# Kernel optimization log

Measured on AMD Instinct MI355X. Metric: run time of the kernel, lower is better.

## Reference

```python
import jax, jax.numpy as jnp
import numpy as np

B, N, D = 1024, 1024, 256


def _mlp(x, w1, b1, w2, b2):
    return jax.nn.relu(x @ w1.T + b1) @ w2.T + b2


def _gru_cell(x, h, wih, whh, bih, bhh):
    gi = x @ wih.T + bih            # [*, 3D]
    gh = h @ whh.T + bhh            # [*, 3D]
    ir, iz, in_ = jnp.split(gi, 3, axis=-1)
    hr, hz, hn = jnp.split(gh, 3, axis=-1)
    r = jax.nn.sigmoid(ir + hr)
    z = jax.nn.sigmoid(iz + hz)
    n = jnp.tanh(in_ + r * hn)
    return (1.0 - z) * n + z * h


def setup_inputs() -> dict:
    key = jax.random.key(0)
    ks = jax.random.split(key, 20)
    s = 0.05
    inp = {
        "memory": jax.random.normal(ks[0], (N, D), jnp.float32),
        "source": jax.random.randint(ks[1], (B, 1), 0, N, jnp.int64 if jax.config.read('jax_enable_x64') else jnp.int32),
        "target": jax.random.randint(ks[2], (B, 1), 0, N, jnp.int64 if jax.config.read('jax_enable_x64') else jnp.int32),
        "delta_t_vec": jax.random.normal(ks[3], (B, N, D), jnp.float32),
        # src_mlp: Linear(3D->D), ReLU, Linear(D->D)
        "src_w1": jax.random.normal(ks[4], (D, 3 * D), jnp.float32) * s,
        "src_b1": jax.random.normal(ks[5], (D,), jnp.float32) * s,
        "src_w2": jax.random.normal(ks[6], (D, D), jnp.float32) * s,
        "src_b2": jax.random.normal(ks[7], (D,), jnp.float32) * s,
        # tar_mlp
        "tar_w1": jax.random.normal(ks[8], (D, 3 * D), jnp.float32) * s,
        "tar_b1": jax.random.normal(ks[9], (D,), jnp.float32) * s,
        "tar_w2": jax.random.normal(ks[10], (D, D), jnp.float32) * s,
        "tar_b2": jax.random.normal(ks[11], (D,), jnp.float32) * s,
        # GRUCell(D, D)
        "gru_wih": jax.random.normal(ks[12], (3 * D, D), jnp.float32) * s,
        "gru_whh": jax.random.normal(ks[13], (3 * D, D), jnp.float32) * s,
        "gru_bih": jax.random.normal(ks[14], (3 * D,), jnp.float32) * s,
        "gru_bhh": jax.random.normal(ks[15], (3 * D,), jnp.float32) * s,
    }
    return inp


def reference(memory, source, target, delta_t_vec,
              src_w1, src_b1, src_w2, src_b2,
              tar_w1, tar_b1, tar_w2, tar_b2,
              gru_wih, gru_whh, gru_bih, gru_bhh):
    b = source.shape[0]
    n_nodes = memory.shape[0]
    src = source[:, 0]
    tgt = target[:, 0]
    bidx = jnp.arange(b)

    src_mem = memory[src]                      # [B,D]
    tgt_mem = memory[tgt]                      # [B,D]
    src_dt = delta_t_vec[bidx, src]            # [B,D]
    tgt_dt = delta_t_vec[bidx, tgt]            # [B,D]

    src_msg = _mlp(jnp.concatenate([src_mem, tgt_mem, src_dt], -1),
                   src_w1, src_b1, src_w2, src_b2)
    tgt_msg = _mlp(jnp.concatenate([tgt_mem, src_mem, tgt_dt], -1),
                   tar_w1, tar_b1, tar_w2, tar_b2)

    # scatter_mean over concatenated (src, tgt) node ids == unique + scatter_mean by inverse index
    nodes = jnp.concatenate([src, tgt], 0)     # [2B]
    msgs = jnp.concatenate([src_msg, tgt_msg], 0)  # [2B,D]
    sums = jax.ops.segment_sum(msgs, nodes, num_segments=n_nodes)      # [N,D]
    cnts = jax.ops.segment_sum(jnp.ones((2 * b,), msgs.dtype), nodes,
                               num_segments=n_nodes)                    # [N]
    agg = sums / jnp.maximum(cnts, 1.0)[:, None]

    new_mem = _gru_cell(agg, memory, gru_wih, gru_whh, gru_bih, gru_bhh)
    touched = (cnts > 0)[:, None]
    return jnp.where(touched, new_mem, memory)
```

## Files before the change

### kernel.cpp

```cpp
#include <hip/hip_runtime.h>
#include <cmath>

typedef unsigned short u16;
typedef unsigned int u32;

using bf16x8 = __attribute__((ext_vector_type(8))) __bf16;
using f32x4  = __attribute__((ext_vector_type(4))) float;

__device__ __forceinline__ u16 f2bf(float f) {
  union { float f; u32 i; } v; v.f = f;
  u32 u = v.i;
  return (u16)((u + 0x7FFFu + ((u >> 16) & 1u)) >> 16);
}

__device__ __forceinline__ uint4 cvt8(const float* __restrict__ p) {
  float4 a = *(const float4*)p;
  float4 b = *(const float4*)(p + 4);
  union { u16 h[8]; uint4 v; } r;
  r.h[0] = f2bf(a.x); r.h[1] = f2bf(a.y); r.h[2] = f2bf(a.z); r.h[3] = f2bf(a.w);
  r.h[4] = f2bf(b.x); r.h[5] = f2bf(b.y); r.h[6] = f2bf(b.z); r.h[7] = f2bf(b.w);
  return r.v;
}
__device__ __forceinline__ uint4 cvt8s(const float* __restrict__ p, float s) {
  float4 a = *(const float4*)p;
  float4 b = *(const float4*)(p + 4);
  union { u16 h[8]; uint4 v; } r;
  r.h[0] = f2bf(a.x * s); r.h[1] = f2bf(a.y * s); r.h[2] = f2bf(a.z * s); r.h[3] = f2bf(a.w * s);
  r.h[4] = f2bf(b.x * s); r.h[5] = f2bf(b.y * s); r.h[6] = f2bf(b.z * s); r.h[7] = f2bf(b.w * s);
  return r.v;
}

#define LDS_STRIDE 72

__global__ __launch_bounds__(256) void k_mlp1(
    const float* __restrict__ memory, const int* __restrict__ src,
    const int* __restrict__ tgt, const float* __restrict__ delta,
    const float* __restrict__ w1s, const float* __restrict__ b1s,
    const float* __restrict__ w1t, const float* __restrict__ b1t,
    u16* __restrict__ H) {
  __shared__ __align__(16) u16 As[64 * LDS_STRIDE];
  __shared__ __align__(16) u16 Bs[64 * LDS_STRIDE];
  const int m0 = blockIdx.x * 64;
  const int n0 = blockIdx.y * 64;
  const int side = (m0 >= 1024);
  const float* __restrict__ W  = side ? w1t : w1s;
  const float* __restrict__ b1 = side ? b1t : b1s;
  const int tid = threadIdx.x;
  const int wv = tid >> 6, lane = tid & 63, quad = lane >> 4, l16 = lane & 15;

  f32x4 acc[4];
#pragma unroll
  for (int i = 0; i < 4; ++i) acc[i] = (f32x4){0.f, 0.f, 0.f, 0.f};

  for (int kc = 0; kc < 768; kc += 64) {
    __syncthreads();
#pragma unroll
    for (int it = 0; it < 2; ++it) {
      int c2 = tid + it * 256;
      int r = c2 >> 3, c8 = (c2 & 7) << 3;
      int k = kc + c8;
      int m = m0 + r, b = m & 1023;
      int ia = side ? tgt[b] : src[b];
      const float* p;
      int seg = k >> 8, kk = k & 255;
      if (seg == 0) {
        p = memory + ia * 256 + kk;
      } else if (seg == 1) {
        int ib = side ? src[b] : tgt[b];
        p = memory + ib * 256 + kk;
      } else {
        p = delta + ((size_t)(b * 1024 + ia)) * 256 + kk;
      }
      *(uint4*)&As[r * LDS_STRIDE + c8] = cvt8(p);
      *(uint4*)&Bs[r * LDS_STRIDE + c8] = cvt8(W + (n0 + r) * 768 + k);
    }
    __syncthreads();
#pragma unroll
    for (int ks = 0; ks < 64; ks += 32) {
      bf16x8 af = *(const bf16x8*)&As[(wv * 16 + l16) * LDS_STRIDE + ks + quad * 8];
#pragma unroll
      for (int nt = 0; nt < 4; ++nt) {
        bf16x8 bf = *(const bf16x8*)&Bs[(nt * 16 + l16) * LDS_STRIDE + ks + quad * 8];
        acc[nt] = __builtin_amdgcn_mfma_f32_16x16x32_bf16(af, bf, acc[nt], 0, 0, 0);
      }
    }
  }
#pragma unroll
  for (int nt = 0; nt < 4; ++nt) {
    int n = n0 + nt * 16 + l16;
    float bias = b1[n];
#pragma unroll
    for (int r = 0; r < 4; ++r) {
      int m = m0 + wv * 16 + quad * 4 + r;
      float v = acc[nt][r] + bias;
      H[m * 256 + n] = f2bf(v > 0.f ? v : 0.f);
    }
  }
}

__global__ __launch_bounds__(256) void k_mlp2_scatter(
    const u16* __restrict__ H, const int* __restrict__ src,
    const int* __restrict__ tgt,
    const float* __restrict__ w2s, const float* __restrict__ b2s,
    const float* __restrict__ w2t, const float* __restrict__ b2t,
    float* __restrict__ sums, float* __restrict__ cnt) {
  __shared__ __align__(16) u16 As[64 * LDS_STRIDE];
  __shared__ __align__(16) u16 Bs[64 * LDS_STRIDE];
  const int m0 = blockIdx.x * 64;
  const int n0 = blockIdx.y * 64;
  const int side = (m0 >= 1024);
  const float* __restrict__ W  = side ? w2t : w2s;
  const float* __restrict__ b2 = side ? b2t : b2s;
  const int tid = threadIdx.x;
  const int wv = tid >> 6, lane = tid & 63, quad = lane >> 4, l16 = lane & 15;

  f32x4 acc[4];
#pragma unroll
  for (int i = 0; i < 4; ++i) acc[i] = (f32x4){0.f, 0.f, 0.f, 0.f};

  for (int kc = 0; kc < 256; kc += 64) {
    __syncthreads();
#pragma unroll
    for (int it = 0; it < 2; ++it) {
      int c2 = tid + it * 256;
      int r = c2 >> 3, c8 = (c2 & 7) << 3;
      int k = kc + c8;
      *(uint4*)&As[r * LDS_STRIDE + c8] = *(const uint4*)(H + (m0 + r) * 256 + k);
      *(uint4*)&Bs[r * LDS_STRIDE + c8] = cvt8(W + (n0 + r) * 256 + k);
    }
    __syncthreads();
#pragma unroll
    for (int ks = 0; ks < 64; ks += 32) {
      bf16x8 af = *(const bf16x8*)&As[(wv * 16 + l16) * LDS_STRIDE + ks + quad * 8];
#pragma unroll
      for (int nt = 0; nt < 4; ++nt) {
        bf16x8 bf = *(const bf16x8*)&Bs[(nt * 16 + l16) * LDS_STRIDE + ks + quad * 8];
        acc[nt] = __builtin_amdgcn_mfma_f32_16x16x32_bf16(af, bf, acc[nt], 0, 0, 0);
      }
    }
  }
#pragma unroll
  for (int nt = 0; nt < 4; ++nt) {
    int n = n0 + nt * 16 + l16;
    float bias = b2[n];
#pragma unroll
    for (int r = 0; r < 4; ++r) {
      int m = m0 + wv * 16 + quad * 4 + r;
      int b = m & 1023;
      int node = side ? tgt[b] : src[b];
      atomicAdd(&sums[node * 256 + n], acc[nt][r] + bias);
    }
  }
  if (blockIdx.y == 0 && l16 == 0) {
#pragma unroll
    for (int r = 0; r < 4; ++r) {
      int m = m0 + wv * 16 + quad * 4 + r;
      int b = m & 1023;
      int node = side ? tgt[b] : src[b];
      atomicAdd(&cnt[node], 1.0f);
    }
  }
}

__global__ __launch_bounds__(256) void k_gru_gemm(
    const float* __restrict__ sums, const float* __restrict__ cnt,
    const float* __restrict__ memory,
    const float* __restrict__ wih, const float* __restrict__ whh,
    const float* __restrict__ bih, const float* __restrict__ bhh,
    float* __restrict__ G) {
  __shared__ __align__(16) u16 As[64 * LDS_STRIDE];
  __shared__ __align__(16) u16 Bs[64 * LDS_STRIDE];
  const int m0 = blockIdx.x * 64;
  const int n0 = blockIdx.y * 64;
  const bool ghreg = (n0 >= 768);
  const int tid = threadIdx.x;
  const int wv = tid >> 6, lane = tid & 63, quad = lane >> 4, l16 = lane & 15;

  f32x4 acc[4];
#pragma unroll
  for (int i = 0; i < 4; ++i) acc[i] = (f32x4){0.f, 0.f, 0.f, 0.f};

  for (int kc = 0; kc < 256; kc += 64) {
    __syncthreads();
#pragma unroll
    for (int it = 0; it < 2; ++it) {
      int c2 = tid + it * 256;
      int r = c2 >> 3, c8 = (c2 & 7) << 3;
      int k = kc + c8;
      int m = m0 + r;
      if (ghreg) {
        *(uint4*)&As[r * LDS_STRIDE + c8] = cvt8(memory + m * 256 + k);
      } else {
        float scale = 1.0f / fmaxf(cnt[m], 1.0f);
        *(uint4*)&As[r * LDS_STRIDE + c8] = cvt8s(sums + m * 256 + k, scale);
      }
      int ng = n0 + r;
      const float* Wr = (ng < 768) ? (wih + ng * 256) : (whh + (ng - 768) * 256);
      *(uint4*)&Bs[r * LDS_STRIDE + c8] = cvt8(Wr + k);
    }
    __syncthreads();
#pragma unroll
    for (int ks = 0; ks < 64; ks += 32) {
      bf16x8 af = *(const bf16x8*)&As[(wv * 16 + l16) * LDS_STRIDE + ks + quad * 8];
#pragma unroll
      for (int nt = 0; nt < 4; ++nt) {
        bf16x8 bf = *(const bf16x8*)&Bs[(nt * 16 + l16) * LDS_STRIDE + ks + quad * 8];
        acc[nt] = __builtin_amdgcn_mfma_f32_16x16x32_bf16(af, bf, acc[nt], 0, 0, 0);
      }
    }
  }
#pragma unroll
  for (int nt = 0; nt < 4; ++nt) {
    int ng = n0 + nt * 16 + l16;
    float bias = (ng < 768) ? bih[ng] : bhh[ng - 768];
#pragma unroll
    for (int r = 0; r < 4; ++r) {
      int m = m0 + wv * 16 + quad * 4 + r;
      G[m * 1536 + ng] = acc[nt][r] + bias;
    }
  }
}

__global__ __launch_bounds__(256) void k_gru_epi(
    const float* __restrict__ G, const float* __restrict__ cnt,
    const float* __restrict__ memory, float* __restrict__ out) {
  int gid = blockIdx.x * 256 + threadIdx.x;
  int m = gid >> 8, d = gid & 255;
  const float* g = G + m * 1536;
  float ir = g[d], iz = g[256 + d], in_ = g[512 + d];
  float hr = g[768 + d], hz = g[1024 + d], hn = g[1280 + d];
  float r = 1.f / (1.f + expf(-(ir + hr)));
  float z = 1.f / (1.f + expf(-(iz + hz)));
  float nn = tanhf(in_ + r * hn);
  float h = memory[gid];
  float nv = (1.f - z) * nn + z * h;
  out[gid] = (cnt[m] > 0.f) ? nv : h;
}

extern "C" void kernel_launch(void* const* d_in, const int* in_sizes, int n_in,
                              void* d_out, int out_size, void* d_ws, size_t ws_size,
                              hipStream_t stream) {
  const float* memory = (const float*)d_in[0];
  const int*   src    = (const int*)d_in[1];
  const int*   tgt    = (const int*)d_in[2];
  const float* delta  = (const float*)d_in[3];
  const float* w1s = (const float*)d_in[4];
  const float* b1s = (const float*)d_in[5];
  const float* w2s = (const float*)d_in[6];
  const float* b2s = (const float*)d_in[7];
  const float* w1t = (const float*)d_in[8];
  const float* b1t = (const float*)d_in[9];
  const float* w2t = (const float*)d_in[10];
  const float* b2t = (const float*)d_in[11];
  const float* wih = (const float*)d_in[12];
  const float* whh = (const float*)d_in[13];
  const float* bih = (const float*)d_in[14];
  const float* bhh = (const float*)d_in[15];

  char* ws = (char*)d_ws;
  float* sums = (float*)ws;
  float* cnt  = (float*)(ws + 1048576);
  u16*   H    = (u16*)(ws + 1052672);
  float* G    = (float*)(ws + 2101248);

  hipMemsetAsync(ws, 0, 1052672, stream);

  k_mlp1<<<dim3(32, 4), 256, 0, stream>>>(memory, src, tgt, delta,
                                          w1s, b1s, w1t, b1t, H);
  k_mlp2_scatter<<<dim3(32, 4), 256, 0, stream>>>(H, src, tgt,
                                                  w2s, b2s, w2t, b2t, sums, cnt);
  k_gru_gemm<<<dim3(16, 24), 256, 0, stream>>>(sums, cnt, memory,
                                               wih, whh, bih, bhh, G);
  k_gru_epi<<<1024, 256, 0, stream>>>(G, cnt, memory, (float*)d_out);
}
```

Measured before the change: 1.215 ms.

## Fuse both message MLP layers and scatter into one kernel with LDS-resident hidden

Merges the first MLP layer kernel and the second-layer-plus-scatter kernel into a single kernel. Each 512-thread block handles 16 rows and all 256 output columns, and keeps the ReLU hidden activations in LDS instead of writing them to a global bf16 buffer. This removes one kernel launch and the global round trip of H. In exchange the grid shrinks from 128 blocks of 256 threads to 128 blocks of 512, each loading the full weight matrices, so weight traffic per row is higher and tiles are smaller (16 rows).

```diff
diff --git a/kernel.cpp b/kernel.cpp
--- a/kernel.cpp
+++ b/kernel.cpp
@@ -31,35 +31,38 @@
 }
 
 #define LDS_STRIDE 72
-
-__global__ __launch_bounds__(256) void k_mlp1(
+#define HS_STRIDE  264
+
+__global__ __launch_bounds__(512) void k_msg_fused(
     const float* __restrict__ memory, const int* __restrict__ src,
     const int* __restrict__ tgt, const float* __restrict__ delta,
     const float* __restrict__ w1s, const float* __restrict__ b1s,
+    const float* __restrict__ w2s, const float* __restrict__ b2s,
     const float* __restrict__ w1t, const float* __restrict__ b1t,
-    u16* __restrict__ H) {
-  __shared__ __align__(16) u16 As[64 * LDS_STRIDE];
-  __shared__ __align__(16) u16 Bs[64 * LDS_STRIDE];
-  const int m0 = blockIdx.x * 64;
-  const int n0 = blockIdx.y * 64;
+    const float* __restrict__ w2t, const float* __restrict__ b2t,
+    float* __restrict__ sums, float* __restrict__ cnt) {
+  __shared__ __align__(16) u16 As[16 * LDS_STRIDE];
+  __shared__ __align__(16) u16 Bs[256 * LDS_STRIDE];
+  __shared__ __align__(16) u16 Hs[16 * HS_STRIDE];
+  const int m0 = blockIdx.x * 16;
   const int side = (m0 >= 1024);
-  const float* __restrict__ W  = side ? w1t : w1s;
-  const float* __restrict__ b1 = side ? b1t : b1s;
+  const float* __restrict__ W1 = side ? w1t : w1s;
+  const float* __restrict__ B1 = side ? b1t : b1s;
+  const float* __restrict__ W2 = side ? w2t : w2s;
+  const float* __restrict__ B2 = side ? b2t : b2s;
   const int tid = threadIdx.x;
   const int wv = tid >> 6, lane = tid & 63, quad = lane >> 4, l16 = lane & 15;
 
-  f32x4 acc[4];
-#pragma unroll
-  for (int i = 0; i < 4; ++i) acc[i] = (f32x4){0.f, 0.f, 0.f, 0.f};
+  f32x4 acc[2];
+#pragma unroll
+  for (int i = 0; i < 2; ++i) acc[i] = (f32x4){0.f, 0.f, 0.f, 0.f};
 
   for (int kc = 0; kc < 768; kc += 64) {
     __syncthreads();
-#pragma unroll
-    for (int it = 0; it < 2; ++it) {
-      int c2 = tid + it * 256;
-      int r = c2 >> 3, c8 = (c2 & 7) << 3;
+    if (tid < 128) {
+      int r = tid >> 3, c8 = (tid & 7) << 3;
       int k = kc + c8;
-      int m = m0 + r, b = m & 1023;
+      int grow = m0 + r, b = grow & 1023;
       int ia = side ? tgt[b] : src[b];
       const float* p;
       int seg = k >> 8, kk = k & 255;
@@ -72,90 +75,72 @@
         p = delta + ((size_t)(b * 1024 + ia)) * 256 + kk;
       }
       *(uint4*)&As[r * LDS_STRIDE + c8] = cvt8(p);
-      *(uint4*)&Bs[r * LDS_STRIDE + c8] = cvt8(W + (n0 + r) * 768 + k);
+    }
+#pragma unroll
+    for (int it = 0; it < 4; ++it) {
+      int c2 = tid + it * 512;
+      int r = c2 >> 3, c8 = (c2 & 7) << 3;
+      *(uint4*)&Bs[r * LDS_STRIDE + c8] = cvt8(W1 + r * 768 + kc + c8);
     }
     __syncthreads();
 #pragma unroll
     for (int ks = 0; ks < 64; ks += 32) {
-      bf16x8 af = *(const bf16x8*)&As[(wv * 16 + l16) * LDS_STRIDE + ks + quad * 8];
-#pragma unroll
-      for (int nt = 0; nt < 4; ++nt) {
-        bf16x8 bf = *(const bf16x8*)&Bs[(nt * 16 + l16) * LDS_STRIDE + ks + quad * 8];
+      bf16x8 af = *(const bf16x8*)&As[l16 * LDS_STRIDE + ks + quad * 8];
+#pragma unroll
+      for (int nt = 0; nt < 2; ++nt) {
+        bf16x8 bf = *(const bf16x8*)&Bs[(wv * 32 + nt * 16 + l16) * LDS_STRIDE + ks + quad * 8];
         acc[nt] = __builtin_amdgcn_mfma_f32_16x16x32_bf16(af, bf, acc[nt], 0, 0, 0);
       }
     }
   }
 #pragma unroll
-  for (int nt = 0; nt < 4; ++nt) {
-    int n = n0 + nt * 16 + l16;
-    float bias = b1[n];
-#pragma unroll
-    for (int r = 0; r < 4; ++r) {
-      int m = m0 + wv * 16 + quad * 4 + r;
+  for (int nt = 0; nt < 2; ++nt) {
+    int n = wv * 32 + nt * 16 + l16;
+    float bias = B1[n];
+#pragma unroll
+    for (int r = 0; r < 4; ++r) {
+      int m = quad * 4 + r;
       float v = acc[nt][r] + bias;
-      H[m * 256 + n] = f2bf(v > 0.f ? v : 0.f);
-    }
-  }
-}
-
-__global__ __launch_bounds__(256) void k_mlp2_scatter(
-    const u16* __restrict__ H, const int* __restrict__ src,
-    const int* __restrict__ tgt,
-    const float* __restrict__ w2s, const float* __restrict__ b2s,
-    const float* __restrict__ w2t, const float* __restrict__ b2t,
-    float* __restrict__ sums, float* __restrict__ cnt) {
-  __shared__ __align__(16) u16 As[64 * LDS_STRIDE];
-  __shared__ __align__(16) u16 Bs[64 * LDS_STRIDE];
-  const int m0 = blockIdx.x * 64;
-  const int n0 = blockIdx.y * 64;
-  const int side = (m0 >= 1024);
-  const float* __restrict__ W  = side ? w2t : w2s;
-  const float* __restrict__ b2 = side ? b2t : b2s;
-  const int tid = threadIdx.x;
-  const int wv = tid >> 6, lane = tid & 63, quad = lane >> 4, l16 = lane & 15;
-
-  f32x4 acc[4];
-#pragma unroll
-  for (int i = 0; i < 4; ++i) acc[i] = (f32x4){0.f, 0.f, 0.f, 0.f};
+      Hs[m * HS_STRIDE + n] = f2bf(v > 0.f ? v : 0.f);
+    }
+    acc[nt] = (f32x4){0.f, 0.f, 0.f, 0.f};
+  }
 
   for (int kc = 0; kc < 256; kc += 64) {
     __syncthreads();
 #pragma unroll
-    for (int it = 0; it < 2; ++it) {
-      int c2 = tid + it * 256;
+    for (int it = 0; it < 4; ++it) {
+      int c2 = tid + it * 512;
       int r = c2 >> 3, c8 = (c2 & 7) << 3;
-      int k = kc + c8;
-      *(uint4*)&As[r * LDS_STRIDE + c8] = *(const uint4*)(H + (m0 + r) * 256 + k);
-      *(uint4*)&Bs[r * LDS_STRIDE + c8] = cvt8(W + (n0 + r) * 256 + k);
+      *(uint4*)&Bs[r * LDS_STRIDE + c8] = cvt8(W2 + r * 256 + kc + c8);
     }
     __syncthreads();
 #pragma unroll
     for (int ks = 0; ks < 64; ks += 32) {
-      bf16x8 af = *(const bf16x8*)&As[(wv * 16 + l16) * LDS_STRIDE + ks + quad * 8];
-#pragma unroll
-      for (int nt = 0; nt < 4; ++nt) {
-        bf16x8 bf = *(const bf16x8*)&Bs[(nt * 16 + l16) * LDS_STRIDE + ks + quad * 8];
+      bf16x8 af = *(const bf16x8*)&Hs[l16 * HS_STRIDE + kc + ks + quad * 8];
+#pragma unroll
+      for (int nt = 0; nt < 2; ++nt) {
+        bf16x8 bf = *(const bf16x8*)&Bs[(wv * 32 + nt * 16 + l16) * LDS_STRIDE + ks + quad * 8];
         acc[nt] = __builtin_amdgcn_mfma_f32_16x16x32_bf16(af, bf, acc[nt], 0, 0, 0);
       }
     }
   }
 #pragma unroll
-  for (int nt = 0; nt < 4; ++nt) {
-    int n = n0 + nt * 16 + l16;
-    float bias = b2[n];
-#pragma unroll
-    for (int r = 0; r < 4; ++r) {
-      int m = m0 + wv * 16 + quad * 4 + r;
-      int b = m & 1023;
+  for (int nt = 0; nt < 2; ++nt) {
+    int n = wv * 32 + nt * 16 + l16;
+    float bias = B2[n];
+#pragma unroll
+    for (int r = 0; r < 4; ++r) {
+      int m = quad * 4 + r;
+      int grow = m0 + m, b = grow & 1023;
       int node = side ? tgt[b] : src[b];
       atomicAdd(&sums[node * 256 + n], acc[nt][r] + bias);
     }
   }
-  if (blockIdx.y == 0 && l16 == 0) {
-#pragma unroll
-    for (int r = 0; r < 4; ++r) {
-      int m = m0 + wv * 16 + quad * 4 + r;
-      int b = m & 1023;
+  if (wv == 0 && l16 == 0) {
+#pragma unroll
+    for (int r = 0; r < 4; ++r) {
+      int grow = m0 + quad * 4 + r, b = grow & 1023;
       int node = side ? tgt[b] : src[b];
       atomicAdd(&cnt[node], 1.0f);
     }
@@ -260,15 +245,13 @@
   char* ws = (char*)d_ws;
   float* sums = (float*)ws;
   float* cnt  = (float*)(ws + 1048576);
-  u16*   H    = (u16*)(ws + 1052672);
-  float* G    = (float*)(ws + 2101248);
+  float* G    = (float*)(ws + 1052672);
 
   hipMemsetAsync(ws, 0, 1052672, stream);
 
-  k_mlp1<<<dim3(32, 4), 256, 0, stream>>>(memory, src, tgt, delta,
-                                          w1s, b1s, w1t, b1t, H);
-  k_mlp2_scatter<<<dim3(32, 4), 256, 0, stream>>>(H, src, tgt,
-                                                  w2s, b2s, w2t, b2t, sums, cnt);
+  k_msg_fused<<<dim3(128), 512, 0, stream>>>(memory, src, tgt, delta,
+                                             w1s, b1s, w2s, b2s,
+                                             w1t, b1t, w2t, b2t, sums, cnt);
   k_gru_gemm<<<dim3(16, 24), 256, 0, stream>>>(sums, cnt, memory,
                                                wih, whh, bih, bhh, G);
   k_gru_epi<<<1024, 256, 0, stream>>>(G, cnt, memory, (float*)d_out);
```

Result: no change. 1.214 ms (-0.0%).
